# Kernel tuning notes

Hardware: AMD Instinct MI355X
Metric: run time of the kernel (lower is better)

## Reference

```python
import jax, jax.numpy as jnp
import numpy as np

GAMMA = 1.4  # adjacency sharpening exponent from TBH


def build_adjacency_hamming(bbn):
    # bbn: [N, D] soft binary codes in [0, 1]
    code_length = jnp.asarray(bbn.shape[1], bbn.dtype)
    m1 = bbn - 1.0
    c = bbn @ m1.T + m1 @ bbn.T            # [N, N]
    normalized_dist = jnp.abs(c) / code_length
    return jnp.power(1.0 - normalized_dist, GAMMA)


def reference(bbn, cbn, W, b):
    adj = build_adjacency_hamming(bbn)      # [N, N], self-connected
    d = jnp.sum(adj, axis=1)                # degree [N]
    d_inv_sqrt = jnp.power(d, -0.5)
    # symmetric normalization D^-1/2 A D^-1/2 without materializing diag matrices
    lap = adj * d_inv_sqrt[:, None] * d_inv_sqrt[None, :]
    h = lap @ cbn                           # [N, cbn_dim] spectral conv
    return jax.nn.sigmoid(h @ W + b)


def setup_inputs() -> dict:
    key = jax.random.key(0)
    k1, k2, k3 = jax.random.split(key, 3)
    N, BBN, CBN = 8192, 64, 512
    bbn = jax.random.uniform(k1, (N, BBN), dtype=jnp.float32)
    cbn = jax.random.normal(k2, (N, CBN), dtype=jnp.float32)
    W = jax.random.normal(k3, (CBN, CBN), dtype=jnp.float32) * (1.0 / np.sqrt(CBN))
    b = jnp.zeros((CBN,), dtype=jnp.float32)
    return {"bbn": bbn, "cbn": cbn, "W": W, "b": b}
```

## Files before the change

### kernel.cpp

```cpp
#include <hip/hip_runtime.h>
#include <hip/hip_bf16.h>

typedef __attribute__((ext_vector_type(8))) short short8;
typedef __attribute__((ext_vector_type(4))) float f32x4;

#define MFMA16(a, b, c) __builtin_amdgcn_mfma_f32_16x16x32_bf16((a), (b), (c), 0, 0, 0)

__device__ __forceinline__ unsigned short f2bf(float x) {
    union { float f; unsigned int u; } v; v.f = x;
    unsigned int u = v.u;
    return (unsigned short)((u + 0x7FFFu + ((u >> 16) & 1u)) >> 16);
}

__device__ __forceinline__ float pow14(float x) {
    return exp2f(1.4f * log2f(x));
}

__device__ __forceinline__ short8 ld8(const unsigned short* p) {
    return *reinterpret_cast<const short8*>(p);
}

__device__ __forceinline__ void gld16(const void* src, const unsigned char* dst) {
    __builtin_amdgcn_global_load_lds(
        (const __attribute__((address_space(1))) void*)src,
        (__attribute__((address_space(3))) void*)dst, 16, 0, 0);
}

__global__ void k_prep_bbn(const float* __restrict__ bbn, unsigned short* __restrict__ bbn_h,
                           unsigned short* __restrict__ bbn_swz, float* __restrict__ s) {
    int row = blockIdx.x * 4 + (threadIdx.x >> 6);
    int lane = threadIdx.x & 63;
    float x = bbn[row * 64 + lane];
    unsigned short h = f2bf(x);
    bbn_h[row * 64 + lane] = h;
    bbn_swz[row * 64 + (lane ^ ((row & 7) << 3))] = h;
    float v = x;
    #pragma unroll
    for (int m = 1; m < 64; m <<= 1) v += __shfl_xor(v, m);
    if (lane == 0) s[row] = v;
}

__global__ void k_zero_d(float* __restrict__ dd) {
    dd[blockIdx.x * 1024 + threadIdx.x] = 0.f;
}

__global__ void k_transpose_scale(const float* __restrict__ in, unsigned short* __restrict__ out,
                                  const float* __restrict__ dvec, int K, int N, int swz) {
    __shared__ float tile[64][65];
    int tiles_k = K >> 6;
    int tk = blockIdx.x % tiles_k, tn = blockIdx.x / tiles_k;
    int k0 = tk * 64, n0 = tn * 64;
    int c = threadIdx.x & 63, rq = threadIdx.x >> 6;
    #pragma unroll
    for (int i = 0; i < 16; ++i) {
        int r = rq + 4 * i;
        float sc = dvec ? rsqrtf(dvec[k0 + r]) : 1.0f;
        tile[r][c] = in[(size_t)(k0 + r) * N + n0 + c] * sc;
    }
    __syncthreads();
    #pragma unroll
    for (int i = 0; i < 16; ++i) {
        int r = rq + 4 * i;
        int cc = swz ? (c ^ ((r & 7) << 3)) : c;
        out[(size_t)(n0 + r) * K + k0 + cc] = f2bf(tile[c][r]);
    }
}

__global__ __launch_bounds__(512, 4) void k_gen_adj(const unsigned short* __restrict__ bbn_h,
                                                    const unsigned short* __restrict__ bbn_swz,
                                                    const float* __restrict__ s,
                                                    unsigned short* __restrict__ A_swz,
                                                    float* __restrict__ dd) {
    int bx = blockIdx.x;
    int it = bx >> 2, jq = bx & 3;
    int i0 = it * 64, jbase = jq * 2048;

    int tid = threadIdx.x;
    int w = tid >> 6, l = tid & 63, g = l >> 4, c = l & 15;
    int gi = w & 3, gj2 = w >> 2;

    const unsigned short* ap = bbn_h + (i0 + gi * 16 + c) * 64;
    short8 ga0 = ld8(ap), ga1 = ld8(ap + 32);
    float si = s[i0 + gi * 16 + c];

    __shared__ unsigned char AjldsF[4 * 8192];
    __shared__ unsigned char OutldsF[2 * 8192];
    __shared__ float sLDS[2048];

    const unsigned short* ajbase = bbn_swz + (jbase + w * 8 + (l >> 3)) * 64 + (l & 7) * 8;
    const int ajdst = w * 1024;

    const int sw = (c & 7) << 4;
    const int gj0 = gj2 * 2, gj1 = gj2 * 2 + 1;
    const int bo00 = (gj0 * 16 + c) * 128 + ((g * 16) ^ sw);
    const int bo01 = (gj0 * 16 + c) * 128 + ((64 + g * 16) ^ sw);
    const int bo10 = (gj1 * 16 + c) * 128 + ((g * 16) ^ sw);
    const int bo11 = (gj1 * 16 + c) * 128 + ((64 + g * 16) ^ sw);
    const int wr0 = ((gi * 16 + c) * 128 + (gj0 * 16 + g * 4) * 2) ^ sw;
    const int wr1 = ((gi * 16 + c) * 128 + (gj1 * 16 + g * 4) * 2) ^ sw;

    float racc = 0.f;

#define GEN_TILE(T, OB) do {                                                       \
    const unsigned char* aj = &AjldsF[((T) & 3) * 8192];                           \
    unsigned char* outp = &OutldsF[(OB) * 8192];                                   \
    _Pragma("unroll")                                                              \
    for (int p = 0; p < 2; ++p) {                                                  \
        short8 gb0 = *reinterpret_cast<const short8*>(&aj[p ? bo10 : bo00]);       \
        short8 gb1 = *reinterpret_cast<const short8*>(&aj[p ? bo11 : bo01]);       \
        f32x4 sj4 = *reinterpret_cast<const f32x4*>(                               \
            &sLDS[(T) * 64 + (p ? gj1 : gj0) * 16 + g * 4]);                       \
        f32x4 gf = {0.f, 0.f, 0.f, 0.f};                                           \
        gf = MFMA16(gb0, ga0, gf);                                                 \
        gf = MFMA16(gb1, ga1, gf);                                                 \
        float t0 = fmaf(2.f, gf[0], -(si + sj4[0]));                               \
        float t1 = fmaf(2.f, gf[1], -(si + sj4[1]));                               \
        float t2 = fmaf(2.f, gf[2], -(si + sj4[2]));                               \
        float t3 = fmaf(2.f, gf[3], -(si + sj4[3]));                               \
        float u0 = pow14(fmaxf(fmaf(fabsf(t0), -0.015625f, 1.f), 0.f));            \
        float u1 = pow14(fmaxf(fmaf(fabsf(t1), -0.015625f, 1.f), 0.f));            \
        float u2 = pow14(fmaxf(fmaf(fabsf(t2), -0.015625f, 1.f), 0.f));            \
        float u3 = pow14(fmaxf(fmaf(fabsf(t3), -0.015625f, 1.f), 0.f));            \
        racc += (u0 + u1) + (u2 + u3);                                             \
        unsigned short p0 = f2bf(u0), p1 = f2bf(u1), p2 = f2bf(u2), p3 = f2bf(u3); \
        *reinterpret_cast<uint2*>(&outp[p ? wr1 : wr0]) =                          \
            make_uint2((unsigned)p0 | ((unsigned)p1 << 16),                        \
                       (unsigned)p2 | ((unsigned)p3 << 16));                       \
    }                                                                              \
} while (0)

#define WB(T, OB) do {                                                             \
    int row_ = tid >> 3, seg_ = tid & 7;                                           \
    uint4 v_ = *reinterpret_cast<const uint4*>(&OutldsF[(OB) * 8192 + tid * 16]);  \
    *reinterpret_cast<uint4*>(A_swz + (size_t)(i0 + row_) * 8192 + jbase + (T) * 64 + seg_ * 8) = v_; \
} while (0)

    gld16(s + jbase + w * 256 + l * 4, (unsigned char*)sLDS + w * 1024);
    gld16(ajbase, &AjldsF[ajdst]);
    gld16(ajbase + 4096, &AjldsF[8192 + ajdst]);
    asm volatile("s_waitcnt vmcnt(0) lgkmcnt(0)\ns_barrier" ::: "memory");

    for (int u = 0; u < 16; ++u) {
        int t2 = (2 * u + 2 < 32) ? 2 * u + 2 : 30;
        int t3 = (2 * u + 3 < 32) ? 2 * u + 3 : 31;
        gld16(ajbase + t2 * 4096, &AjldsF[((2 * u + 2) & 3) * 8192 + ajdst]);
        gld16(ajbase + t3 * 4096, &AjldsF[((2 * u + 3) & 3) * 8192 + ajdst]);
        if (u > 0) { WB(2 * u - 2, 0); WB(2 * u - 1, 1); }
        GEN_TILE(2 * u, 0);
        GEN_TILE(2 * u + 1, 1);
        asm volatile("s_waitcnt vmcnt(2) lgkmcnt(0)\ns_barrier" ::: "memory");
    }
    WB(30, 0);
    WB(31, 1);
#undef GEN_TILE
#undef WB

    racc += __shfl_xor(racc, 16);
    racc += __shfl_xor(racc, 32);
    if (g == 0) atomicAdd(&dd[i0 + gi * 16 + c], racc);
}

__global__ __launch_bounds__(512, 4) void k_spectral(const unsigned short* __restrict__ A_swz,
                                                     const unsigned short* __restrict__ cbn_sT,
                                                     float* __restrict__ hpart) {
    int bx = blockIdx.x;
    int row = bx >> 2, ks = bx & 3;
    int i0 = row * 64, k0 = ks * 2048;

    int tid = threadIdx.x;
    int w = tid >> 6, l = tid & 63, g = l >> 4, c = l & 15;
    int lrow = l >> 3, lseg = l & 7;

    __shared__ unsigned char Alds[8192];
    __shared__ unsigned char Blds[65536];

    f32x4 acc[4][4] = {};

    const unsigned short* srcA = A_swz + (size_t)(i0 + w * 8 + lrow) * 8192 + k0 + lseg * 8;
    const unsigned short* srcB = cbn_sT + (size_t)(w * 8 + lrow) * 8192 + k0 + lseg * 8;
    const int sw = (c & 7) << 4;

    for (int t = 0; t < 32; ++t) {
        int jt = t * 64;
        gld16(srcA + jt, &Alds[w * 1024]);
        #pragma unroll
        for (int q = 0; q < 8; ++q)
            gld16(srcB + (size_t)(q * 64) * 8192 + jt, &Blds[(q * 64 + w * 8) * 128]);
        asm volatile("s_waitcnt vmcnt(0) lgkmcnt(0)\ns_barrier" ::: "memory");

        #pragma unroll
        for (int kk = 0; kk < 2; ++kk) {
            short8 af[4], bf[4];
            #pragma unroll
            for (int mi = 0; mi < 4; ++mi)
                af[mi] = *reinterpret_cast<const short8*>(
                    &Alds[(mi * 16 + c) * 128 + ((kk * 64 + g * 16) ^ sw)]);
            #pragma unroll
            for (int nn = 0; nn < 4; ++nn)
                bf[nn] = *reinterpret_cast<const short8*>(
                    &Blds[(w * 64 + nn * 16 + c) * 128 + ((kk * 64 + g * 16) ^ sw)]);
            __builtin_amdgcn_s_setprio(1);
            #pragma unroll
            for (int mi = 0; mi < 4; ++mi)
                #pragma unroll
                for (int nn = 0; nn < 4; ++nn)
                    acc[mi][nn] = MFMA16(af[mi], bf[nn], acc[mi][nn]);
            __builtin_amdgcn_s_setprio(0);
        }
        asm volatile("s_waitcnt lgkmcnt(0)\ns_barrier" ::: "memory");
    }

    float* hp = hpart + (size_t)bx * 32768;
    #pragma unroll
    for (int mi = 0; mi < 4; ++mi)
        #pragma unroll
        for (int r = 0; r < 4; ++r) {
            int lr = mi * 16 + g * 4 + r;
            #pragma unroll
            for (int nn = 0; nn < 4; ++nn)
                hp[lr * 512 + w * 64 + nn * 16 + c] = acc[mi][nn][r];
        }
}

__global__ __launch_bounds__(256) void k_reduce(const float* __restrict__ hpart,
                                                const float* __restrict__ dd,
                                                unsigned short* __restrict__ h) {
    size_t flat = ((size_t)blockIdx.x * 256 + threadIdx.x) * 4;
    int i = (int)(flat >> 9), n = (int)(flat & 511);
    int row = i >> 6;
    int local = (i & 63) * 512 + n;
    size_t base = (size_t)(row * 4) * 32768;
    f32x4 v0 = *reinterpret_cast<const f32x4*>(hpart + base + local);
    f32x4 v1 = *reinterpret_cast<const f32x4*>(hpart + base + 32768 + local);
    f32x4 v2 = *reinterpret_cast<const f32x4*>(hpart + base + 2 * 32768 + local);
    f32x4 v3 = *reinterpret_cast<const f32x4*>(hpart + base + 3 * 32768 + local);
    f32x4 sum = (v0 + v1) + (v2 + v3);
    float dinv = rsqrtf(dd[i]);
    ushort4 o;
    o.x = f2bf(sum[0] * dinv);
    o.y = f2bf(sum[1] * dinv);
    o.z = f2bf(sum[2] * dinv);
    o.w = f2bf(sum[3] * dinv);
    *reinterpret_cast<ushort4*>(h + flat) = o;
}

__global__ __launch_bounds__(512) void k_out(const unsigned short* __restrict__ h,
                                             const unsigned short* __restrict__ Wt,
                                             const float* __restrict__ b,
                                             float* __restrict__ out) {
    int bx = blockIdx.x;
    int i0 = (bx & 255) * 32, n0 = (bx >> 8) * 256;
    int tid = threadIdx.x;
    int w = tid >> 6, l = tid & 63, g = l >> 4, c = l & 15;
    int wm = w >> 2, wn = w & 3;

    float bb[4];
    #pragma unroll
    for (int nn = 0; nn < 4; ++nn) bb[nn] = b[n0 + wn * 64 + nn * 16 + c];

    f32x4 acc[4] = {};
    for (int k0 = 0; k0 < 512; k0 += 64) {
        short8 af[2];
        #pragma unroll
        for (int kk = 0; kk < 2; ++kk)
            af[kk] = ld8(h + (size_t)(i0 + wm * 16 + c) * 512 + k0 + kk * 32 + g * 8);
        #pragma unroll
        for (int kk = 0; kk < 2; ++kk)
            #pragma unroll
            for (int nn = 0; nn < 4; ++nn) {
                short8 bf = ld8(Wt + (size_t)(n0 + wn * 64 + nn * 16 + c) * 512 + k0 + kk * 32 + g * 8);
                acc[nn] = MFMA16(af[kk], bf, acc[nn]);
            }
    }
    #pragma unroll
    for (int r = 0; r < 4; ++r) {
        int row = i0 + wm * 16 + g * 4 + r;
        #pragma unroll
        for (int nn = 0; nn < 4; ++nn) {
            float z = acc[nn][r] + bb[nn];
            out[(size_t)row * 512 + n0 + wn * 64 + nn * 16 + c] = 1.f / (1.f + exp2f(-1.44269504f * z));
        }
    }
}

extern "C" void kernel_launch(void* const* d_in, const int* in_sizes, int n_in,
                              void* d_out, int out_size, void* d_ws, size_t ws_size,
                              hipStream_t stream) {
    const float* bbn = (const float*)d_in[0];
    const float* cbn = (const float*)d_in[1];
    const float* W   = (const float*)d_in[2];
    const float* b   = (const float*)d_in[3];
    float* out = (float*)d_out;

    char* ws = (char*)d_ws;
    unsigned short* bbn_h   = (unsigned short*)(ws);
    unsigned short* bbn_swz = (unsigned short*)(ws + (1u << 20));
    float*          s       = (float*)(ws + (2u << 20));
    float*          dd      = (float*)(ws + (2u << 20) + (1u << 15));
    unsigned short* Wt      = (unsigned short*)(ws + (2u << 20) + (2u << 15));
    unsigned short* cbn_sT  = (unsigned short*)(ws + (3u << 20));
    unsigned short* hbuf    = (unsigned short*)(ws + (11u << 20));
    unsigned short* A_swz   = (unsigned short*)(ws + (19u << 20));
    float*          hpart   = (float*)(ws + (147u << 20));

    k_prep_bbn<<<2048, 256, 0, stream>>>(bbn, bbn_h, bbn_swz, s);
    k_zero_d<<<8, 1024, 0, stream>>>(dd);
    k_transpose_scale<<<64, 256, 0, stream>>>(W, Wt, nullptr, 512, 512, 0);
    k_gen_adj<<<512, 512, 0, stream>>>(bbn_h, bbn_swz, s, A_swz, dd);
    k_transpose_scale<<<1024, 256, 0, stream>>>(cbn, cbn_sT, dd, 8192, 512, 1);
    k_spectral<<<512, 512, 0, stream>>>(A_swz, cbn_sT, hpart);
    k_reduce<<<4096, 256, 0, stream>>>(hpart, dd, hbuf);
    k_out<<<512, 512, 0, stream>>>(hbuf, Wt, b, out);
}
```

Before: 195.3 us.

## Exploit adjacency symmetry: compute upper-triangle tiles and mirror-store transposes

The adjacency generator now launches one 64x64 block per upper-triangular tile pair (ti<=tj), found by inverting the triangular index, instead of streaming full row strips. Each off-diagonal tile is written twice, once directly and once transposed through LDS. Row and column degree partials go to a per-tile buffer that a new reduction kernel sums, replacing the atomics and the zeroing kernel. This roughly halves the MFMA and pow work, but adds uncoalesced transposed writes built from scalar 2-byte LDS reads, extra shuffles, and many short-lived blocks with no intra-block pipelining.

```diff
diff --git a/kernel.cpp b/kernel.cpp
--- a/kernel.cpp
+++ b/kernel.cpp
@@ -40,10 +40,6 @@
     if (lane == 0) s[row] = v;
 }
 
-__global__ void k_zero_d(float* __restrict__ dd) {
-    dd[blockIdx.x * 1024 + threadIdx.x] = 0.f;
-}
-
 __global__ void k_transpose_scale(const float* __restrict__ in, unsigned short* __restrict__ out,
                                   const float* __restrict__ dvec, int K, int N, int swz) {
     __shared__ float tile[64][65];
@@ -66,98 +62,134 @@
     }
 }
 
-__global__ __launch_bounds__(512, 4) void k_gen_adj(const unsigned short* __restrict__ bbn_h,
+__global__ __launch_bounds__(256, 4) void k_gen_adj(const unsigned short* __restrict__ bbn_h,
                                                     const unsigned short* __restrict__ bbn_swz,
                                                     const float* __restrict__ s,
                                                     unsigned short* __restrict__ A_swz,
-                                                    float* __restrict__ dd) {
+                                                    float* __restrict__ dpart) {
     int bx = blockIdx.x;
-    int it = bx >> 2, jq = bx & 3;
-    int i0 = it * 64, jbase = jq * 2048;
+    int ti = (int)((257.0f - sqrtf(66049.0f - 8.0f * (float)bx)) * 0.5f);
+    while (ti * (257 - ti) / 2 > bx) --ti;
+    while ((ti + 1) * (256 - ti) / 2 <= bx) ++ti;
+    int tj = ti + (bx - ti * (257 - ti) / 2);
+    int i0 = ti * 64, jbase = tj * 64;
 
     int tid = threadIdx.x;
     int w = tid >> 6, l = tid & 63, g = l >> 4, c = l & 15;
-    int gi = w & 3, gj2 = w >> 2;
-
-    const unsigned short* ap = bbn_h + (i0 + gi * 16 + c) * 64;
+
+    __shared__ __align__(16) unsigned char Ajlds[8192];
+    __shared__ __align__(16) unsigned char Outlds[8192];
+    __shared__ float colbuf[4][64];
+
+    gld16(bbn_swz + (jbase + w * 8 + (l >> 3)) * 64 + (l & 7) * 8, &Ajlds[w * 1024]);
+    gld16(bbn_swz + (jbase + 32 + w * 8 + (l >> 3)) * 64 + (l & 7) * 8, &Ajlds[4096 + w * 1024]);
+
+    const unsigned short* ap = bbn_h + (i0 + w * 16 + c) * 64;
     short8 ga0 = ld8(ap), ga1 = ld8(ap + 32);
-    float si = s[i0 + gi * 16 + c];
-
-    __shared__ unsigned char AjldsF[4 * 8192];
-    __shared__ unsigned char OutldsF[2 * 8192];
-    __shared__ float sLDS[2048];
-
-    const unsigned short* ajbase = bbn_swz + (jbase + w * 8 + (l >> 3)) * 64 + (l & 7) * 8;
-    const int ajdst = w * 1024;
+    float si = s[i0 + w * 16 + c];
+    f32x4 sj4_0 = *reinterpret_cast<const f32x4*>(s + jbase + 0 * 16 + g * 4);
+    f32x4 sj4_1 = *reinterpret_cast<const f32x4*>(s + jbase + 1 * 16 + g * 4);
+    f32x4 sj4_2 = *reinterpret_cast<const f32x4*>(s + jbase + 2 * 16 + g * 4);
+    f32x4 sj4_3 = *reinterpret_cast<const f32x4*>(s + jbase + 3 * 16 + g * 4);
+
+    asm volatile("s_waitcnt vmcnt(0) lgkmcnt(0)\ns_barrier" ::: "memory");
 
     const int sw = (c & 7) << 4;
-    const int gj0 = gj2 * 2, gj1 = gj2 * 2 + 1;
-    const int bo00 = (gj0 * 16 + c) * 128 + ((g * 16) ^ sw);
-    const int bo01 = (gj0 * 16 + c) * 128 + ((64 + g * 16) ^ sw);
-    const int bo10 = (gj1 * 16 + c) * 128 + ((g * 16) ^ sw);
-    const int bo11 = (gj1 * 16 + c) * 128 + ((64 + g * 16) ^ sw);
-    const int wr0 = ((gi * 16 + c) * 128 + (gj0 * 16 + g * 4) * 2) ^ sw;
-    const int wr1 = ((gi * 16 + c) * 128 + (gj1 * 16 + g * 4) * 2) ^ sw;
-
     float racc = 0.f;
 
-#define GEN_TILE(T, OB) do {                                                       \
-    const unsigned char* aj = &AjldsF[((T) & 3) * 8192];                           \
-    unsigned char* outp = &OutldsF[(OB) * 8192];                                   \
-    _Pragma("unroll")                                                              \
-    for (int p = 0; p < 2; ++p) {                                                  \
-        short8 gb0 = *reinterpret_cast<const short8*>(&aj[p ? bo10 : bo00]);       \
-        short8 gb1 = *reinterpret_cast<const short8*>(&aj[p ? bo11 : bo01]);       \
-        f32x4 sj4 = *reinterpret_cast<const f32x4*>(                               \
-            &sLDS[(T) * 64 + (p ? gj1 : gj0) * 16 + g * 4]);                       \
-        f32x4 gf = {0.f, 0.f, 0.f, 0.f};                                           \
-        gf = MFMA16(gb0, ga0, gf);                                                 \
-        gf = MFMA16(gb1, ga1, gf);                                                 \
-        float t0 = fmaf(2.f, gf[0], -(si + sj4[0]));                               \
-        float t1 = fmaf(2.f, gf[1], -(si + sj4[1]));                               \
-        float t2 = fmaf(2.f, gf[2], -(si + sj4[2]));                               \
-        float t3 = fmaf(2.f, gf[3], -(si + sj4[3]));                               \
-        float u0 = pow14(fmaxf(fmaf(fabsf(t0), -0.015625f, 1.f), 0.f));            \
-        float u1 = pow14(fmaxf(fmaf(fabsf(t1), -0.015625f, 1.f), 0.f));            \
-        float u2 = pow14(fmaxf(fmaf(fabsf(t2), -0.015625f, 1.f), 0.f));            \
-        float u3 = pow14(fmaxf(fmaf(fabsf(t3), -0.015625f, 1.f), 0.f));            \
-        racc += (u0 + u1) + (u2 + u3);                                             \
-        unsigned short p0 = f2bf(u0), p1 = f2bf(u1), p2 = f2bf(u2), p3 = f2bf(u3); \
-        *reinterpret_cast<uint2*>(&outp[p ? wr1 : wr0]) =                          \
-            make_uint2((unsigned)p0 | ((unsigned)p1 << 16),                        \
-                       (unsigned)p2 | ((unsigned)p3 << 16));                       \
+#define GEN_SUB(GJ, SJ4) do {                                                      \
+    short8 gb0 = *reinterpret_cast<const short8*>(                                 \
+        &Ajlds[((GJ) * 16 + c) * 128 + ((g * 16) ^ sw)]);                          \
+    short8 gb1 = *reinterpret_cast<const short8*>(                                 \
+        &Ajlds[((GJ) * 16 + c) * 128 + ((64 + g * 16) ^ sw)]);                     \
+    f32x4 gf = {0.f, 0.f, 0.f, 0.f};                                               \
+    gf = MFMA16(gb0, ga0, gf);                                                     \
+    gf = MFMA16(gb1, ga1, gf);                                                     \
+    float t0 = fmaf(2.f, gf[0], -(si + (SJ4)[0]));                                 \
+    float t1 = fmaf(2.f, gf[1], -(si + (SJ4)[1]));                                 \
+    float t2 = fmaf(2.f, gf[2], -(si + (SJ4)[2]));                                 \
+    float t3 = fmaf(2.f, gf[3], -(si + (SJ4)[3]));                                 \
+    float u0 = pow14(fmaxf(fmaf(fabsf(t0), -0.015625f, 1.f), 0.f));                \
+    float u1 = pow14(fmaxf(fmaf(fabsf(t1), -0.015625f, 1.f), 0.f));                \
+    float u2 = pow14(fmaxf(fmaf(fabsf(t2), -0.015625f, 1.f), 0.f));                \
+    float u3 = pow14(fmaxf(fmaf(fabsf(t3), -0.015625f, 1.f), 0.f));                \
+    racc += (u0 + u1) + (u2 + u3);                                                 \
+    if (ti != tj) {      \
+        float s0 = u0, s1 = u1, s2 = u2, s3 = u3;                                  \
+        s0 += __shfl_xor(s0, 1); s0 += __shfl_xor(s0, 2);                          \
+        s0 += __shfl_xor(s0, 4); s0 += __shfl_xor(s0, 8);                          \
+        s1 += __shfl_xor(s1, 1); s1 += __shfl_xor(s1, 2);                          \
+        s1 += __shfl_xor(s1, 4); s1 += __shfl_xor(s1, 8);                          \
+        s2 += __shfl_xor(s2, 1); s2 += __shfl_xor(s2, 2);                          \
+        s2 += __shfl_xor(s2, 4); s2 += __shfl_xor(s2, 8);                          \
+        s3 += __shfl_xor(s3, 1); s3 += __shfl_xor(s3, 2);                          \
+        s3 += __shfl_xor(s3, 4); s3 += __shfl_xor(s3, 8);                          \
+        if (c == 0) {                                                              \
+            f32x4 cs = {s0, s1, s2, s3};                                           \
+            *reinterpret_cast<f32x4*>(&colbuf[w][(GJ) * 16 + g * 4]) = cs;         \
+        }                                                                          \
     }                                                                              \
+    unsigned short p0 = f2bf(u0), p1 = f2bf(u1), p2 = f2bf(u2), p3 = f2bf(u3);     \
+    *reinterpret_cast<uint2*>(                                                     \
+        &Outlds[(((w * 16 + c) * 128 + ((GJ) * 16 + g * 4) * 2) ^ sw)]) =          \
+        make_uint2((unsigned)p0 | ((unsigned)p1 << 16),                            \
+                   (unsigned)p2 | ((unsigned)p3 << 16));                           \
 } while (0)
 
-#define WB(T, OB) do {                                                             \
-    int row_ = tid >> 3, seg_ = tid & 7;                                           \
-    uint4 v_ = *reinterpret_cast<const uint4*>(&OutldsF[(OB) * 8192 + tid * 16]);  \
-    *reinterpret_cast<uint4*>(A_swz + (size_t)(i0 + row_) * 8192 + jbase + (T) * 64 + seg_ * 8) = v_; \
-} while (0)
-
-    gld16(s + jbase + w * 256 + l * 4, (unsigned char*)sLDS + w * 1024);
-    gld16(ajbase, &AjldsF[ajdst]);
-    gld16(ajbase + 4096, &AjldsF[8192 + ajdst]);
-    asm volatile("s_waitcnt vmcnt(0) lgkmcnt(0)\ns_barrier" ::: "memory");
-
-    for (int u = 0; u < 16; ++u) {
-        int t2 = (2 * u + 2 < 32) ? 2 * u + 2 : 30;
-        int t3 = (2 * u + 3 < 32) ? 2 * u + 3 : 31;
-        gld16(ajbase + t2 * 4096, &AjldsF[((2 * u + 2) & 3) * 8192 + ajdst]);
-        gld16(ajbase + t3 * 4096, &AjldsF[((2 * u + 3) & 3) * 8192 + ajdst]);
-        if (u > 0) { WB(2 * u - 2, 0); WB(2 * u - 1, 1); }
-        GEN_TILE(2 * u, 0);
-        GEN_TILE(2 * u + 1, 1);
-        asm volatile("s_waitcnt vmcnt(2) lgkmcnt(0)\ns_barrier" ::: "memory");
-    }
-    WB(30, 0);
-    WB(31, 1);
-#undef GEN_TILE
-#undef WB
+    GEN_SUB(0, sj4_0);
+    GEN_SUB(1, sj4_1);
+    GEN_SUB(2, sj4_2);
+    GEN_SUB(3, sj4_3);
+#undef GEN_SUB
 
     racc += __shfl_xor(racc, 16);
     racc += __shfl_xor(racc, 32);
-    if (g == 0) atomicAdd(&dd[i0 + gi * 16 + c], racc);
+    if (g == 0) dpart[(size_t)tj * 8192 + i0 + w * 16 + c] = racc;
+
+    asm volatile("s_waitcnt lgkmcnt(0)\ns_barrier" ::: "memory");
+
+    if (ti != tj && tid < 64) {
+        float v = colbuf[0][tid] + colbuf[1][tid] + colbuf[2][tid] + colbuf[3][tid];
+        dpart[(size_t)ti * 8192 + jbase + tid] = v;
+    }
+
+    {
+        int row = tid >> 2, seg = tid & 3;
+        uint4 v0 = *reinterpret_cast<const uint4*>(&Outlds[tid * 32]);
+        uint4 v1 = *reinterpret_cast<const uint4*>(&Outlds[tid * 32 + 16]);
+        unsigned short* dst = A_swz + (size_t)(i0 + row) * 8192 + jbase + seg * 16;
+        *reinterpret_cast<uint4*>(dst) = v0;
+        *reinterpret_cast<uint4*>(dst + 8) = v1;
+    }
+    if (ti != tj) {
+        int jt = tid >> 2, grp = tid & 3;
+        int Xj = (jt & 7) << 3;
+        #pragma unroll
+        for (int hh = 0; hh < 2; ++hh) {
+            unsigned short vv[8];
+            #pragma unroll
+            for (int e = 0; e < 8; ++e) {
+                int it = grp * 16 + hh * 8 + e;
+                vv[e] = *reinterpret_cast<const unsigned short*>(
+                    &Outlds[it * 128 + ((jt * 2) ^ ((it & 7) << 4))]);
+            }
+            uint4 pk = make_uint4(
+                (unsigned)vv[0] | ((unsigned)vv[1] << 16),
+                (unsigned)vv[2] | ((unsigned)vv[3] << 16),
+                (unsigned)vv[4] | ((unsigned)vv[5] << 16),
+                (unsigned)vv[6] | ((unsigned)vv[7] << 16));
+            *reinterpret_cast<uint4*>(
+                A_swz + (size_t)(jbase + jt) * 8192 + i0 + ((grp * 16 + hh * 8) ^ Xj)) = pk;
+        }
+    }
+}
+
+__global__ __launch_bounds__(256) void k_degree_sum(const float* __restrict__ dpart,
+                                                    float* __restrict__ dd) {
+    int i = blockIdx.x * 256 + threadIdx.x;
+    float v = 0.f;
+    for (int cb = 0; cb < 128; ++cb) v += dpart[(size_t)cb * 8192 + i];
+    dd[i] = v;
 }
 
 __global__ __launch_bounds__(512, 4) void k_spectral(const unsigned short* __restrict__ A_swz,
@@ -302,11 +334,12 @@
     unsigned short* hbuf    = (unsigned short*)(ws + (11u << 20));
     unsigned short* A_swz   = (unsigned short*)(ws + (19u << 20));
     float*          hpart   = (float*)(ws + (147u << 20));
+    float*          dpart   = (float*)(ws + (211u << 20));
 
     k_prep_bbn<<<2048, 256, 0, stream>>>(bbn, bbn_h, bbn_swz, s);
-    k_zero_d<<<8, 1024, 0, stream>>>(dd);
     k_transpose_scale<<<64, 256, 0, stream>>>(W, Wt, nullptr, 512, 512, 0);
-    k_gen_adj<<<512, 512, 0, stream>>>(bbn_h, bbn_swz, s, A_swz, dd);
+    k_gen_adj<<<8256, 256, 0, stream>>>(bbn_h, bbn_swz, s, A_swz, dpart);
+    k_degree_sum<<<32, 256, 0, stream>>>(dpart, dd);
     k_transpose_scale<<<1024, 256, 0, stream>>>(cbn, cbn_sT, dd, 8192, 512, 1);
     k_spectral<<<512, 512, 0, stream>>>(A_swz, cbn_sT, hpart);
     k_reduce<<<4096, 256, 0, stream>>>(hpart, dd, hbuf);
```

Result: no change. 198.6 us (+1.7%).
